# Optimization experiments

Measured on AMD Instinct MI355X. Metric: run time of the kernel, lower is better.

Reference implementation:

```python
import jax, jax.numpy as jnp
import numpy as np

B, S, D, H = 4, 2048, 1024, 16
DH = D // H
DFF = 4 * D
EPS = 1e-7


def _layernorm(x, scale, shift):
    # Note original quirk: (normalized + shift) * scale, biased variance, eps=1e-7
    m = jnp.mean(x, axis=-1, keepdims=True)
    v = jnp.mean((x - m) ** 2, axis=-1, keepdims=True)
    return ((x - m) / jnp.sqrt(v + EPS) + shift) * scale


def _gelu(x):
    c = jnp.sqrt(jnp.asarray(2.0 / jnp.pi, dtype=x.dtype))
    return 0.5 * x * (1.0 + jnp.tanh(c * (x + 0.044715 * x ** 3)))


def setup_inputs() -> dict:
    key = jax.random.key(0)
    ks = jax.random.split(key, 8)
    s = 0.02
    return {
        "x": jax.random.normal(ks[0], (B, S, D), jnp.float32),
        "Wq": jax.random.normal(ks[1], (D, D), jnp.float32) * s,
        "Wk": jax.random.normal(ks[2], (D, D), jnp.float32) * s,
        "Wv": jax.random.normal(ks[3], (D, D), jnp.float32) * s,
        "Wo": jax.random.normal(ks[4], (D, D), jnp.float32) * s,
        "bo": jnp.zeros((D,), jnp.float32),
        "W1": jax.random.normal(ks[5], (DFF, D), jnp.float32) * s,
        "b1": jnp.zeros((DFF,), jnp.float32),
        "W2": jax.random.normal(ks[6], (D, DFF), jnp.float32) * s,
        "b2": jnp.zeros((D,), jnp.float32),
        "ln1_scale": jnp.ones((D,), jnp.float32),
        "ln1_shift": jnp.zeros((D,), jnp.float32),
        "ln2_scale": jnp.ones((D,), jnp.float32),
        "ln2_shift": jnp.zeros((D,), jnp.float32),
    }


def reference(x, Wq, Wk, Wv, Wo, bo, W1, b1, W2, b2,
              ln1_scale, ln1_shift, ln2_scale, ln2_shift):
    b, s, d = x.shape
    h = _layernorm(x, ln1_scale, ln1_shift)
    # torch Linear: y = h @ W.T
    q = (h @ Wq.T).reshape(b, s, H, DH).transpose(0, 2, 1, 3)  # bhsd
    k = (h @ Wk.T).reshape(b, s, H, DH).transpose(0, 2, 1, 3)
    v = (h @ Wv.T).reshape(b, s, H, DH).transpose(0, 2, 1, 3)
    scores = jnp.einsum('bhqd,bhkd->bhqk', q, k) / jnp.sqrt(jnp.asarray(DH, x.dtype))
    causal = jnp.tril(jnp.ones((s, s), dtype=bool))
    scores = jnp.where(causal, scores, -jnp.inf)
    attn = jax.nn.softmax(scores, axis=-1)
    ctx = jnp.einsum('bhqk,bhkd->bhqd', attn, v)
    ctx = ctx.transpose(0, 2, 1, 3).reshape(b, s, d)
    attn_out = ctx @ Wo.T + bo
    x1 = x + attn_out  # residual (dropout is identity at eval / p effectively unused)
    h2 = _layernorm(x1, ln2_scale, ln2_shift)
    ff = _gelu(h2 @ W1.T + b1) @ W2.T + b2
    return x1 + ff
```

## Files before the change

kernel.cpp:

```cpp
#include <hip/hip_runtime.h>
#include <hip/hip_bf16.h>
#include <math.h>

typedef __bf16 bf16;
typedef __bf16 bf16x2_t __attribute__((ext_vector_type(2)));
typedef __bf16 bf16x4_t __attribute__((ext_vector_type(4)));
typedef __bf16 bf16x8_t __attribute__((ext_vector_type(8)));
typedef float  floatx4  __attribute__((ext_vector_type(4)));

#define DEVI static __device__ __forceinline__

constexpr int Bb = 4, Ss = 2048, Dd = 1024, Hh = 16, DHh = 64, DFFc = 4096;
constexpr int NTOK = Bb * Ss;
constexpr int NQKV = 3072;

DEVI void gld_lds16(const void* g, void* l) {
  __builtin_amdgcn_global_load_lds(
      (const __attribute__((address_space(1))) void*)g,
      (__attribute__((address_space(3))) void*)l, 16, 0, 0);
}

DEVI float gelu_f(float x) {
  const float c = 0.7978845608028654f;
  float t = tanhf(c * (x + 0.044715f * x * x * x));
  return 0.5f * x * (1.0f + t);
}

DEVI int xcd_lin(int lin, int nwg) {
  return (lin & 7) * (nwg >> 3) + (lin >> 3);
}

struct CastArgs {
  const float* src[6];
  bf16* dst[6];
  int n[6];
};
__global__ __launch_bounds__(256) void cast_w_kernel(CastArgs a) {
  const int which = blockIdx.y;
  const int idx = (blockIdx.x * 256 + threadIdx.x) * 4;
  if (idx >= a.n[which]) return;
  float4 v = *(const float4*)(a.src[which] + idx);
  bf16x4_t o = {(bf16)v.x, (bf16)v.y, (bf16)v.z, (bf16)v.w};
  *(bf16x4_t*)(a.dst[which] + idx) = o;
}

template <typename TIN>
__global__ __launch_bounds__(256) void ln_kernel(const TIN* __restrict__ x,
                                                 const float* __restrict__ sc,
                                                 const float* __restrict__ sh,
                                                 bf16* __restrict__ out) {
  __shared__ float rs[4], rs2[4];
  const int row = blockIdx.x, t = threadIdx.x;
  const TIN* xr = x + (size_t)row * Dd;
  float v[4];
  if constexpr (sizeof(TIN) == 2) {
    bf16x4_t tmp = *(const bf16x4_t*)((const bf16*)xr + t * 4);
#pragma unroll
    for (int i = 0; i < 4; i++) v[i] = (float)tmp[i];
  } else {
    float4 tmp = *(const float4*)((const float*)xr + t * 4);
    v[0] = tmp.x; v[1] = tmp.y; v[2] = tmp.z; v[3] = tmp.w;
  }
  float s = v[0] + v[1] + v[2] + v[3];
  float s2 = v[0] * v[0] + v[1] * v[1] + v[2] * v[2] + v[3] * v[3];
#pragma unroll
  for (int off = 1; off < 64; off <<= 1) {
    s += __shfl_xor(s, off);
    s2 += __shfl_xor(s2, off);
  }
  if ((t & 63) == 0) { rs[t >> 6] = s; rs2[t >> 6] = s2; }
  __syncthreads();
  float S1 = rs[0] + rs[1] + rs[2] + rs[3];
  float S2 = rs2[0] + rs2[1] + rs2[2] + rs2[3];
  float mean = S1 * (1.0f / Dd);
  float var = S2 * (1.0f / Dd) - mean * mean;
  float rinv = rsqrtf(var + 1e-7f);
#pragma unroll
  for (int i = 0; i < 4; i++) {
    int c = t * 4 + i;
    out[(size_t)row * Dd + c] = (bf16)(((v[i] - mean) * rinv + sh[c]) * sc[c]);
  }
}

template <int BN, int MODE>
__global__ __launch_bounds__(512, 2) void gemm8(const bf16* __restrict__ A,
                                                const bf16* __restrict__ Bw,
                                                const float* __restrict__ bias,
                                                const void* __restrict__ res,
                                                void* __restrict__ outp,
                                                int M, int N, int K) {
  constexpr int WARPS_N = (BN == 256) ? 4 : 2;
  constexpr int WR_H = (BN == 256) ? 128 : 64;
  constexpr int M_rep = WR_H / 16;
  constexpr int MPP = M_rep / 4;
  constexpr int NBCH = BN / 128;
  constexpr int BELEM = BN * 64;
  __shared__ bf16 lds[32768 + 2 * BELEM];

  const int tid = threadIdx.x;
  const int w = tid >> 6, lane = tid & 63;
  const int quad = lane >> 4, l16 = lane & 15;
  const int l7x8 = (lane & 7) << 3;
  const int wr = w / WARPS_N, wc = w % WARPS_N;

  const int gx = (int)gridDim.x;
  const int nwg = gx * (int)gridDim.y;
  const int lin = xcd_lin((int)blockIdx.y * gx + (int)blockIdx.x, nwg);
  const int m0 = (lin / gx) * 256;
  const int n0 = (lin % gx) * BN;

  const int s0 = w * 1024 + lane * 16;
  const int sr = s0 >> 7;
  const int sc = ((s0 ^ ((sr & 7) << 4)) & 127) >> 1;
  const int toff = w * 512 + lane * 8;

  const bf16* Ag[2][2];
  const bf16* Bg[NBCH][2];
#pragma unroll
  for (int h = 0; h < 2; h++)
#pragma unroll
    for (int j = 0; j < 2; j++)
      Ag[h][j] = A + (size_t)(m0 + h * 128 + sr + j * 64) * K + sc;
#pragma unroll
  for (int h = 0; h < NBCH; h++)
#pragma unroll
    for (int j = 0; j < 2; j++)
      Bg[h][j] = Bw + (size_t)(n0 + h * 128 + sr + j * 64) * K + sc;

  const int abase = (wr * WR_H + l16) * 64 + quad * 8;
  const int bbase = (wc * 64 + l16) * 64 + quad * 8;

  floatx4 acc[M_rep][4] = {};

#pragma unroll
  for (int h = 0; h < 2; h++)
#pragma unroll
    for (int j = 0; j < 2; j++)
      gld_lds16(Ag[h][j], lds + h * 8192 + j * 4096 + toff);
#pragma unroll
  for (int h = 0; h < NBCH; h++)
#pragma unroll
    for (int j = 0; j < 2; j++)
      gld_lds16(Bg[h][j], lds + 32768 + h * 8192 + j * 4096 + toff);
  asm volatile("s_waitcnt vmcnt(0)" ::: "memory");
  __builtin_amdgcn_s_barrier();
  __builtin_amdgcn_sched_barrier(0);

  const int NT = K >> 6;
  int koff = 64;
  for (int t = 0; t < NT; ++t) {
    const int q = t & 1;
    const int aq = q * 16384;
    const int bq = 32768 + q * BELEM;
    const int aqn = (q ^ 1) * 16384;
    const int bqn = 32768 + (q ^ 1) * BELEM;
    const bool st = (t + 1) < NT;

    bf16x8_t bfr[4][2];
#pragma unroll
    for (int p = 0; p < 4; ++p) {
      if (st) {
        if (p == 0) {
#pragma unroll
          for (int j = 0; j < 2; j++)
            gld_lds16(Ag[0][j] + koff, lds + aqn + j * 4096 + toff);
#pragma unroll
          for (int j = 0; j < 2; j++)
            gld_lds16(Bg[0][j] + koff, lds + bqn + j * 4096 + toff);
        }
        if (p == 1) {
#pragma unroll
          for (int j = 0; j < 2; j++)
            gld_lds16(Ag[1][j] + koff, lds + aqn + 8192 + j * 4096 + toff);
        }
        if (p == 2 && NBCH == 2) {
#pragma unroll
          for (int j = 0; j < 2; j++)
            gld_lds16(Bg[1][j] + koff, lds + bqn + 8192 + j * 4096 + toff);
        }
      }
      bf16x8_t af[MPP][2];
#pragma unroll
      for (int im = 0; im < MPP; ++im)
#pragma unroll
        for (int kk = 0; kk < 2; ++kk)
          af[im][kk] = *(const bf16x8_t*)(
              lds + aq + ((abase + (p * MPP + im) * 1024 + kk * 32) ^ l7x8));
      if (p == 0) {
#pragma unroll
        for (int j2 = 0; j2 < 4; ++j2)
#pragma unroll
          for (int kk = 0; kk < 2; ++kk)
            bfr[j2][kk] = *(const bf16x8_t*)(
                lds + bq + ((bbase + j2 * 1024 + kk * 32) ^ l7x8));
      }
      __builtin_amdgcn_s_barrier();
      __builtin_amdgcn_sched_barrier(0);
      __builtin_amdgcn_s_setprio(1);
#pragma unroll
      for (int im = 0; im < MPP; ++im)
#pragma unroll
        for (int j2 = 0; j2 < 4; ++j2)
#pragma unroll
          for (int kk = 0; kk < 2; ++kk)
            acc[p * MPP + im][j2] = __builtin_amdgcn_mfma_f32_16x16x32_bf16(
                af[im][kk], bfr[j2][kk], acc[p * MPP + im][j2], 0, 0, 0);
      __builtin_amdgcn_s_setprio(0);
      if (p < 3) {
        __builtin_amdgcn_s_barrier();
        __builtin_amdgcn_sched_barrier(0);
      }
    }
    asm volatile("s_waitcnt vmcnt(0)" ::: "memory");
    __builtin_amdgcn_sched_barrier(0);
    __builtin_amdgcn_s_barrier();
    __builtin_amdgcn_sched_barrier(0);
    if (st) koff += 64;
  }

#pragma unroll
  for (int i = 0; i < M_rep; ++i) {
    const int rbase = m0 + wr * WR_H + i * 16 + quad * 4;
#pragma unroll
    for (int j2 = 0; j2 < 4; ++j2) {
      const int col = n0 + wc * 64 + j2 * 16 + l16;
      float bv = 0.f;
      if constexpr (MODE == 1 || MODE == 2 || MODE == 3) bv = bias[col];
#pragma unroll
      for (int r = 0; r < 4; ++r) {
        const int row = rbase + r;
        float vacc = acc[i][j2][r] + bv;
        if constexpr (MODE == 0) {
          ((bf16*)outp)[(size_t)row * N + col] = (bf16)vacc;
        } else if constexpr (MODE == 1) {
          float xres = ((const float*)res)[(size_t)row * N + col];
          ((bf16*)outp)[(size_t)row * N + col] = (bf16)(xres + vacc);
        } else if constexpr (MODE == 2) {
          ((bf16*)outp)[(size_t)row * N + col] = (bf16)gelu_f(vacc);
        } else {
          float xres = (float)((const bf16*)res)[(size_t)row * N + col];
          ((float*)outp)[(size_t)row * N + col] = xres + vacc;
        }
      }
    }
  }
}

__global__ __launch_bounds__(256) void attn_kernel(const bf16* __restrict__ QKV,
                                                   bf16* __restrict__ ctx) {
  __shared__ bf16 Ks[64 * 72];
  __shared__ bf16 Vt[64 * 72];
  __shared__ bf16 Ps[4][16 * 72];

  const int tid = threadIdx.x;
  const int wave = tid >> 6, lane = tid & 63;
  const int quad = lane >> 4, l16 = lane & 15;
  const int lin = xcd_lin((int)blockIdx.y * 16 + (int)blockIdx.x, 16 * Bb * Hh);
  const int qb = lin & 15;
  const int bh = lin >> 4;
  const int bsel = bh >> 4, hsel = bh & 15;
  const size_t base = ((size_t)bsel * Ss) * NQKV + (size_t)hsel * 64;
  const bf16* Qp = QKV + base;
  const bf16* Kp = QKV + base + 1024;
  const bf16* Vp = QKV + base + 2048;

  const int kr0 = tid >> 3, kc0 = (tid & 7) * 8;
  const int vp2 = tid & 31, vs = tid >> 5;

  for (int t = 0; t < 2; t++) {
    const int qt = (t == 0) ? qb : 31 - qb;
    const int q0 = qt * 64;

    const int qrow = q0 + wave * 16 + l16;
    bf16x8_t qf0 = *(const bf16x8_t*)(Qp + (size_t)qrow * NQKV + quad * 8);
    bf16x8_t qf1 = *(const bf16x8_t*)(Qp + (size_t)qrow * NQKV + 32 + quad * 8);
#pragma unroll
    for (int i = 0; i < 8; i++) {
      qf0[i] = (bf16)((float)qf0[i] * 0.125f);
      qf1[i] = (bf16)((float)qf1[i] * 0.125f);
    }

    floatx4 o[4] = {};
    float l_i[4] = {0.f, 0.f, 0.f, 0.f};

    for (int kc = 0; kc < q0 + 64; kc += 64) {
      __syncthreads();
      *(bf16x8_t*)(Ks + kr0 * 72 + kc0) =
          *(const bf16x8_t*)(Kp + (size_t)(kc + kr0) * NQKV + kc0);
      *(bf16x8_t*)(Ks + (kr0 + 32) * 72 + kc0) =
          *(const bf16x8_t*)(Kp + (size_t)(kc + kr0 + 32) * NQKV + kc0);
      {
        const bf16* v0p = Vp + (size_t)(kc + 2 * vp2) * NQKV + vs * 8;
        bf16x8_t va = *(const bf16x8_t*)(v0p);
        bf16x8_t vb = *(const bf16x8_t*)(v0p + NQKV);
#pragma unroll
        for (int i = 0; i < 8; i++) {
          bf16x2_t p2 = {va[i], vb[i]};
          *(bf16x2_t*)(Vt + (vs * 8 + i) * 72 + 2 * vp2) = p2;
        }
      }
      __syncthreads();

      floatx4 sg[4];
      __builtin_amdgcn_s_setprio(1);
#pragma unroll
      for (int g = 0; g < 4; g++) {
        floatx4 s = {0.f, 0.f, 0.f, 0.f};
        bf16x8_t ka = *(const bf16x8_t*)(Ks + (g * 16 + l16) * 72 + quad * 8);
        bf16x8_t kb = *(const bf16x8_t*)(Ks + (g * 16 + l16) * 72 + 32 + quad * 8);
        s = __builtin_amdgcn_mfma_f32_16x16x32_bf16(qf0, ka, s, 0, 0, 0);
        s = __builtin_amdgcn_mfma_f32_16x16x32_bf16(qf1, kb, s, 0, 0, 0);
        sg[g] = s;
      }
      __builtin_amdgcn_s_setprio(0);

      bf16* pw = &Ps[wave][0];
#pragma unroll
      for (int r = 0; r < 4; r++) {
        const int rq = q0 + wave * 16 + quad * 4 + r;
        float p[4];
        float rsum = 0.f;
#pragma unroll
        for (int g = 0; g < 4; g++) {
          float v = (kc + g * 16 + l16 > rq) ? -1e30f : sg[g][r];
          p[g] = __expf(v);
          rsum += p[g];
        }
        rsum += __shfl_xor(rsum, 1);
        rsum += __shfl_xor(rsum, 2);
        rsum += __shfl_xor(rsum, 4);
        rsum += __shfl_xor(rsum, 8);
        l_i[r] += rsum;
#pragma unroll
        for (int g = 0; g < 4; g++)
          pw[(quad * 4 + r) * 72 + g * 16 + l16] = (bf16)p[g];
      }
      __syncthreads();

      bf16x8_t pf0 = *(const bf16x8_t*)(pw + l16 * 72 + quad * 8);
      bf16x8_t pf1 = *(const bf16x8_t*)(pw + l16 * 72 + 32 + quad * 8);
      __builtin_amdgcn_s_setprio(1);
#pragma unroll
      for (int nt = 0; nt < 4; nt++) {
        bf16x8_t vf0 = *(const bf16x8_t*)(Vt + (nt * 16 + l16) * 72 + quad * 8);
        bf16x8_t vf1 = *(const bf16x8_t*)(Vt + (nt * 16 + l16) * 72 + 32 + quad * 8);
        o[nt] = __builtin_amdgcn_mfma_f32_16x16x32_bf16(pf0, vf0, o[nt], 0, 0, 0);
        o[nt] = __builtin_amdgcn_mfma_f32_16x16x32_bf16(pf1, vf1, o[nt], 0, 0, 0);
      }
      __builtin_amdgcn_s_setprio(0);
    }

#pragma unroll
    for (int nt = 0; nt < 4; nt++)
#pragma unroll
      for (int r = 0; r < 4; r++) {
        const int rq = q0 + wave * 16 + quad * 4 + r;
        size_t a = ((size_t)bsel * Ss + rq) * Dd + (size_t)hsel * DHh + nt * 16 + l16;
        ctx[a] = (bf16)(o[nt][r] / l_i[r]);
      }
  }
}

extern "C" void kernel_launch(void* const* d_in, const int* in_sizes, int n_in,
                              void* d_out, int out_size, void* d_ws, size_t ws_size,
                              hipStream_t stream) {
  (void)in_sizes; (void)n_in; (void)out_size; (void)ws_size;
  const float* x = (const float*)d_in[0];
  const float* Wq = (const float*)d_in[1];
  const float* Wk = (const float*)d_in[2];
  const float* Wv = (const float*)d_in[3];
  const float* Wo = (const float*)d_in[4];
  const float* bo = (const float*)d_in[5];
  const float* W1 = (const float*)d_in[6];
  const float* b1 = (const float*)d_in[7];
  const float* W2 = (const float*)d_in[8];
  const float* b2 = (const float*)d_in[9];
  const float* ln1s = (const float*)d_in[10];
  const float* ln1b = (const float*)d_in[11];
  const float* ln2s = (const float*)d_in[12];
  const float* ln2b = (const float*)d_in[13];

  char* wsb = (char*)d_ws;
  const size_t MB = 1024 * 1024;
  bf16* Wqb = (bf16*)(wsb);
  bf16* Wkb = (bf16*)(wsb + 2 * MB);
  bf16* Wvb = (bf16*)(wsb + 4 * MB);
  bf16* Wob = (bf16*)(wsb + 6 * MB);
  bf16* W1b = (bf16*)(wsb + 8 * MB);
  bf16* W2b = (bf16*)(wsb + 16 * MB);
  bf16* h   = (bf16*)(wsb + 24 * MB);
  bf16* qkv = (bf16*)(wsb + 40 * MB);
  bf16* ctx = (bf16*)(wsb + 88 * MB);
  bf16* x1  = (bf16*)(wsb + 104 * MB);
  bf16* h2  = ctx;
  bf16* ff1 = h;

  dim3 blk(256, 1, 1);
  dim3 blk8(512, 1, 1);

  CastArgs ca;
  ca.src[0] = Wq; ca.src[1] = Wk; ca.src[2] = Wv; ca.src[3] = Wo;
  ca.src[4] = W1; ca.src[5] = W2;
  ca.dst[0] = Wqb; ca.dst[1] = Wkb; ca.dst[2] = Wvb; ca.dst[3] = Wob;
  ca.dst[4] = W1b; ca.dst[5] = W2b;
  ca.n[0] = ca.n[1] = ca.n[2] = ca.n[3] = Dd * Dd;
  ca.n[4] = ca.n[5] = Dd * DFFc;
  cast_w_kernel<<<dim3((Dd * DFFc) / (256 * 4), 6, 1), blk, 0, stream>>>(ca);

  ln_kernel<float><<<dim3(NTOK, 1, 1), blk, 0, stream>>>(x, ln1s, ln1b, h);
  gemm8<128, 0><<<dim3(24, NTOK / 256, 1), blk8, 0, stream>>>(h, Wqb, nullptr, nullptr,
                                                              qkv, NTOK, NQKV, Dd);
  attn_kernel<<<dim3(16, Bb * Hh, 1), blk, 0, stream>>>(qkv, ctx);
  gemm8<128, 1><<<dim3(8, NTOK / 256, 1), blk8, 0, stream>>>(ctx, Wob, bo, x, x1,
                                                             NTOK, Dd, Dd);
  ln_kernel<bf16><<<dim3(NTOK, 1, 1), blk, 0, stream>>>(x1, ln2s, ln2b, h2);
  gemm8<256, 2><<<dim3(16, NTOK / 256, 1), blk8, 0, stream>>>(h2, W1b, b1, nullptr, ff1,
                                                              NTOK, DFFc, Dd);
  gemm8<128, 3><<<dim3(8, NTOK / 256, 1), blk8, 0, stream>>>(ff1, W2b, b2, x1,
                                                             (float*)d_out, NTOK, Dd, DFFc);
}
```

Measured before the change: 521.9 us.

## Triple-buffer GEMM k-loop and prefetch next K/V tile in attention

The GEMM moves to a three-stage LDS ring buffer with a fixed 256x128 tile, issuing loads two k-steps ahead and waiting with a partial vmcnt instead of draining every iteration. The FF1 GEMM now uses this narrower tile too. In attention, the next K/V tile is loaded into registers while the current tile computes, and the causal mask is applied only on the diagonal tile. The larger LDS footprint can lower blocks per CU.

```diff
diff --git a/kernel.cpp b/kernel.cpp
--- a/kernel.cpp
+++ b/kernel.cpp
@@ -82,32 +82,30 @@
   }
 }
 
-template <int BN, int MODE>
+template <int MODE>
 __global__ __launch_bounds__(512, 2) void gemm8(const bf16* __restrict__ A,
                                                 const bf16* __restrict__ Bw,
                                                 const float* __restrict__ bias,
                                                 const void* __restrict__ res,
                                                 void* __restrict__ outp,
                                                 int M, int N, int K) {
-  constexpr int WARPS_N = (BN == 256) ? 4 : 2;
-  constexpr int WR_H = (BN == 256) ? 128 : 64;
-  constexpr int M_rep = WR_H / 16;
-  constexpr int MPP = M_rep / 4;
-  constexpr int NBCH = BN / 128;
-  constexpr int BELEM = BN * 64;
-  __shared__ bf16 lds[32768 + 2 * BELEM];
+  constexpr int ABUF = 16384;
+  constexpr int BBUF = 8192;
+  __shared__ bf16 lds[3 * (ABUF + BBUF)];
+  bf16* Ab = lds;
+  bf16* Bb = lds + 3 * ABUF;
 
   const int tid = threadIdx.x;
   const int w = tid >> 6, lane = tid & 63;
   const int quad = lane >> 4, l16 = lane & 15;
   const int l7x8 = (lane & 7) << 3;
-  const int wr = w / WARPS_N, wc = w % WARPS_N;
+  const int wr = w >> 1, wc = w & 1;
 
   const int gx = (int)gridDim.x;
   const int nwg = gx * (int)gridDim.y;
   const int lin = xcd_lin((int)blockIdx.y * gx + (int)blockIdx.x, nwg);
   const int m0 = (lin / gx) * 256;
-  const int n0 = (lin % gx) * BN;
+  const int n0 = (lin % gx) * 128;
 
   const int s0 = w * 1024 + lane * 16;
   const int sr = s0 >> 7;
@@ -115,112 +113,90 @@
   const int toff = w * 512 + lane * 8;
 
   const bf16* Ag[2][2];
-  const bf16* Bg[NBCH][2];
+  const bf16* Bg[2];
 #pragma unroll
   for (int h = 0; h < 2; h++)
 #pragma unroll
     for (int j = 0; j < 2; j++)
-      Ag[h][j] = A + (size_t)(m0 + h * 128 + sr + j * 64) * K + sc;
-#pragma unroll
-  for (int h = 0; h < NBCH; h++)
+      Ag[h][j] = A + (size_t)(m0 + h * 128 + j * 64 + sr) * K + sc;
+#pragma unroll
+  for (int j = 0; j < 2; j++)
+    Bg[j] = Bw + (size_t)(n0 + j * 64 + sr) * K + sc;
+
+  auto issue = [&](int kofs, int s) {
+#pragma unroll
+    for (int h = 0; h < 2; h++)
+#pragma unroll
+      for (int j = 0; j < 2; j++)
+        gld_lds16(Ag[h][j] + kofs, Ab + s * ABUF + h * 8192 + j * 4096 + toff);
 #pragma unroll
     for (int j = 0; j < 2; j++)
-      Bg[h][j] = Bw + (size_t)(n0 + h * 128 + sr + j * 64) * K + sc;
-
-  const int abase = (wr * WR_H + l16) * 64 + quad * 8;
+      gld_lds16(Bg[j] + kofs, Bb + s * BBUF + j * 4096 + toff);
+  };
+
+  const int abase = (wr * 64 + l16) * 64 + quad * 8;
   const int bbase = (wc * 64 + l16) * 64 + quad * 8;
 
-  floatx4 acc[M_rep][4] = {};
-
-#pragma unroll
-  for (int h = 0; h < 2; h++)
-#pragma unroll
-    for (int j = 0; j < 2; j++)
-      gld_lds16(Ag[h][j], lds + h * 8192 + j * 4096 + toff);
-#pragma unroll
-  for (int h = 0; h < NBCH; h++)
-#pragma unroll
-    for (int j = 0; j < 2; j++)
-      gld_lds16(Bg[h][j], lds + 32768 + h * 8192 + j * 4096 + toff);
-  asm volatile("s_waitcnt vmcnt(0)" ::: "memory");
-  __builtin_amdgcn_s_barrier();
-  __builtin_amdgcn_sched_barrier(0);
+  floatx4 acc[4][4] = {};
 
   const int NT = K >> 6;
-  int koff = 64;
+  issue(0, 0);
+  issue(64, 1);
+
   for (int t = 0; t < NT; ++t) {
-    const int q = t & 1;
-    const int aq = q * 16384;
-    const int bq = 32768 + q * BELEM;
-    const int aqn = (q ^ 1) * 16384;
-    const int bqn = 32768 + (q ^ 1) * BELEM;
-    const bool st = (t + 1) < NT;
-
+    const int s = t % 3;
+    if (t < NT - 1) {
+      asm volatile("s_waitcnt vmcnt(6)" ::: "memory");
+    } else {
+      asm volatile("s_waitcnt vmcnt(0)" ::: "memory");
+    }
+    __builtin_amdgcn_sched_barrier(0);
+    __builtin_amdgcn_s_barrier();
+    __builtin_amdgcn_sched_barrier(0);
+    if (t + 2 < NT) issue((t + 2) * 64, (t + 2) % 3);
+
+    const bf16* aB = Ab + s * ABUF;
+    const bf16* bB = Bb + s * BBUF;
     bf16x8_t bfr[4][2];
 #pragma unroll
-    for (int p = 0; p < 4; ++p) {
-      if (st) {
-        if (p == 0) {
-#pragma unroll
-          for (int j = 0; j < 2; j++)
-            gld_lds16(Ag[0][j] + koff, lds + aqn + j * 4096 + toff);
-#pragma unroll
-          for (int j = 0; j < 2; j++)
-            gld_lds16(Bg[0][j] + koff, lds + bqn + j * 4096 + toff);
-        }
-        if (p == 1) {
-#pragma unroll
-          for (int j = 0; j < 2; j++)
-            gld_lds16(Ag[1][j] + koff, lds + aqn + 8192 + j * 4096 + toff);
-        }
-        if (p == 2 && NBCH == 2) {
-#pragma unroll
-          for (int j = 0; j < 2; j++)
-            gld_lds16(Bg[1][j] + koff, lds + bqn + 8192 + j * 4096 + toff);
-        }
-      }
-      bf16x8_t af[MPP][2];
-#pragma unroll
-      for (int im = 0; im < MPP; ++im)
+    for (int p = 0; p < 2; ++p) {
+      bf16x8_t af[2][2];
+#pragma unroll
+      for (int im = 0; im < 2; ++im)
 #pragma unroll
         for (int kk = 0; kk < 2; ++kk)
           af[im][kk] = *(const bf16x8_t*)(
-              lds + aq + ((abase + (p * MPP + im) * 1024 + kk * 32) ^ l7x8));
+              aB + ((abase + (p * 2 + im) * 1024 + kk * 32) ^ l7x8));
       if (p == 0) {
 #pragma unroll
         for (int j2 = 0; j2 < 4; ++j2)
 #pragma unroll
           for (int kk = 0; kk < 2; ++kk)
             bfr[j2][kk] = *(const bf16x8_t*)(
-                lds + bq + ((bbase + j2 * 1024 + kk * 32) ^ l7x8));
+                bB + ((bbase + j2 * 1024 + kk * 32) ^ l7x8));
       }
       __builtin_amdgcn_s_barrier();
       __builtin_amdgcn_sched_barrier(0);
       __builtin_amdgcn_s_setprio(1);
 #pragma unroll
-      for (int im = 0; im < MPP; ++im)
+      for (int im = 0; im < 2; ++im)
 #pragma unroll
         for (int j2 = 0; j2 < 4; ++j2)
 #pragma unroll
           for (int kk = 0; kk < 2; ++kk)
-            acc[p * MPP + im][j2] = __builtin_amdgcn_mfma_f32_16x16x32_bf16(
-                af[im][kk], bfr[j2][kk], acc[p * MPP + im][j2], 0, 0, 0);
+            acc[p * 2 + im][j2] = __builtin_amdgcn_mfma_f32_16x16x32_bf16(
+                af[im][kk], bfr[j2][kk], acc[p * 2 + im][j2], 0, 0, 0);
       __builtin_amdgcn_s_setprio(0);
-      if (p < 3) {
+      if (p == 0) {
         __builtin_amdgcn_s_barrier();
         __builtin_amdgcn_sched_barrier(0);
       }
     }
-    asm volatile("s_waitcnt vmcnt(0)" ::: "memory");
-    __builtin_amdgcn_sched_barrier(0);
-    __builtin_amdgcn_s_barrier();
-    __builtin_amdgcn_sched_barrier(0);
-    if (st) koff += 64;
-  }
-
-#pragma unroll
-  for (int i = 0; i < M_rep; ++i) {
-    const int rbase = m0 + wr * WR_H + i * 16 + quad * 4;
+  }
+
+#pragma unroll
+  for (int i = 0; i < 4; ++i) {
+    const int rbase = m0 + wr * 64 + i * 16 + quad * 4;
 #pragma unroll
     for (int j2 = 0; j2 < 4; ++j2) {
       const int col = n0 + wc * 64 + j2 * 16 + l16;
@@ -283,23 +259,36 @@
     floatx4 o[4] = {};
     float l_i[4] = {0.f, 0.f, 0.f, 0.f};
 
-    for (int kc = 0; kc < q0 + 64; kc += 64) {
+    {
+      bf16x8_t k0 = *(const bf16x8_t*)(Kp + (size_t)kr0 * NQKV + kc0);
+      bf16x8_t k1 = *(const bf16x8_t*)(Kp + (size_t)(kr0 + 32) * NQKV + kc0);
+      const bf16* v0p = Vp + (size_t)(2 * vp2) * NQKV + vs * 8;
+      bf16x8_t va = *(const bf16x8_t*)(v0p);
+      bf16x8_t vb = *(const bf16x8_t*)(v0p + NQKV);
+      *(bf16x8_t*)(Ks + kr0 * 72 + kc0) = k0;
+      *(bf16x8_t*)(Ks + (kr0 + 32) * 72 + kc0) = k1;
+#pragma unroll
+      for (int i = 0; i < 8; i++) {
+        bf16x2_t p2 = {va[i], vb[i]};
+        *(bf16x2_t*)(Vt + (vs * 8 + i) * 72 + 2 * vp2) = p2;
+      }
       __syncthreads();
-      *(bf16x8_t*)(Ks + kr0 * 72 + kc0) =
-          *(const bf16x8_t*)(Kp + (size_t)(kc + kr0) * NQKV + kc0);
-      *(bf16x8_t*)(Ks + (kr0 + 32) * 72 + kc0) =
-          *(const bf16x8_t*)(Kp + (size_t)(kc + kr0 + 32) * NQKV + kc0);
-      {
-        const bf16* v0p = Vp + (size_t)(kc + 2 * vp2) * NQKV + vs * 8;
-        bf16x8_t va = *(const bf16x8_t*)(v0p);
-        bf16x8_t vb = *(const bf16x8_t*)(v0p + NQKV);
-#pragma unroll
-        for (int i = 0; i < 8; i++) {
-          bf16x2_t p2 = {va[i], vb[i]};
-          *(bf16x2_t*)(Vt + (vs * 8 + i) * 72 + 2 * vp2) = p2;
-        }
-      }
-      __syncthreads();
+    }
+
+    const int ntiles = qt + 1;
+    for (int it = 0; it < ntiles; ++it) {
+      const int kc = it * 64;
+      const bool more = (it + 1) < ntiles;
+
+      bf16x8_t nk0, nk1, nva, nvb;
+      if (more) {
+        const int kn = kc + 64;
+        nk0 = *(const bf16x8_t*)(Kp + (size_t)(kn + kr0) * NQKV + kc0);
+        nk1 = *(const bf16x8_t*)(Kp + (size_t)(kn + kr0 + 32) * NQKV + kc0);
+        const bf16* v0p = Vp + (size_t)(kn + 2 * vp2) * NQKV + vs * 8;
+        nva = *(const bf16x8_t*)(v0p);
+        nvb = *(const bf16x8_t*)(v0p + NQKV);
+      }
 
       floatx4 sg[4];
       __builtin_amdgcn_s_setprio(1);
@@ -315,27 +304,48 @@
       __builtin_amdgcn_s_setprio(0);
 
       bf16* pw = &Ps[wave][0];
-#pragma unroll
-      for (int r = 0; r < 4; r++) {
-        const int rq = q0 + wave * 16 + quad * 4 + r;
-        float p[4];
-        float rsum = 0.f;
-#pragma unroll
-        for (int g = 0; g < 4; g++) {
-          float v = (kc + g * 16 + l16 > rq) ? -1e30f : sg[g][r];
-          p[g] = __expf(v);
-          rsum += p[g];
+      const bool diag = (kc == q0);
+      if (diag) {
+#pragma unroll
+        for (int r = 0; r < 4; r++) {
+          const int rq = q0 + wave * 16 + quad * 4 + r;
+          float p[4];
+          float rsum = 0.f;
+#pragma unroll
+          for (int g = 0; g < 4; g++) {
+            float v = (kc + g * 16 + l16 > rq) ? -1e30f : sg[g][r];
+            p[g] = __expf(v);
+            rsum += p[g];
+          }
+          rsum += __shfl_xor(rsum, 1);
+          rsum += __shfl_xor(rsum, 2);
+          rsum += __shfl_xor(rsum, 4);
+          rsum += __shfl_xor(rsum, 8);
+          l_i[r] += rsum;
+#pragma unroll
+          for (int g = 0; g < 4; g++)
+            pw[(quad * 4 + r) * 72 + g * 16 + l16] = (bf16)p[g];
         }
-        rsum += __shfl_xor(rsum, 1);
-        rsum += __shfl_xor(rsum, 2);
-        rsum += __shfl_xor(rsum, 4);
-        rsum += __shfl_xor(rsum, 8);
-        l_i[r] += rsum;
-#pragma unroll
-        for (int g = 0; g < 4; g++)
-          pw[(quad * 4 + r) * 72 + g * 16 + l16] = (bf16)p[g];
-      }
-      __syncthreads();
+      } else {
+#pragma unroll
+        for (int r = 0; r < 4; r++) {
+          float p[4];
+          float rsum = 0.f;
+#pragma unroll
+          for (int g = 0; g < 4; g++) {
+            p[g] = __expf(sg[g][r]);
+            rsum += p[g];
+          }
+          rsum += __shfl_xor(rsum, 1);
+          rsum += __shfl_xor(rsum, 2);
+          rsum += __shfl_xor(rsum, 4);
+          rsum += __shfl_xor(rsum, 8);
+          l_i[r] += rsum;
+#pragma unroll
+          for (int g = 0; g < 4; g++)
+            pw[(quad * 4 + r) * 72 + g * 16 + l16] = (bf16)p[g];
+        }
+      }
 
       bf16x8_t pf0 = *(const bf16x8_t*)(pw + l16 * 72 + quad * 8);
       bf16x8_t pf1 = *(const bf16x8_t*)(pw + l16 * 72 + 32 + quad * 8);
@@ -348,6 +358,18 @@
         o[nt] = __builtin_amdgcn_mfma_f32_16x16x32_bf16(pf1, vf1, o[nt], 0, 0, 0);
       }
       __builtin_amdgcn_s_setprio(0);
+
+      __syncthreads();
+      if (more) {
+        *(bf16x8_t*)(Ks + kr0 * 72 + kc0) = nk0;
+        *(bf16x8_t*)(Ks + (kr0 + 32) * 72 + kc0) = nk1;
+#pragma unroll
+        for (int i = 0; i < 8; i++) {
+          bf16x2_t p2 = {nva[i], nvb[i]};
+          *(bf16x2_t*)(Vt + (vs * 8 + i) * 72 + 2 * vp2) = p2;
+        }
+        __syncthreads();
+      }
     }
 
 #pragma unroll
@@ -408,14 +430,14 @@
   cast_w_kernel<<<dim3((Dd * DFFc) / (256 * 4), 6, 1), blk, 0, stream>>>(ca);
 
   ln_kernel<float><<<dim3(NTOK, 1, 1), blk, 0, stream>>>(x, ln1s, ln1b, h);
-  gemm8<128, 0><<<dim3(24, NTOK / 256, 1), blk8, 0, stream>>>(h, Wqb, nullptr, nullptr,
-                                                              qkv, NTOK, NQKV, Dd);
+  gemm8<0><<<dim3(24, NTOK / 256, 1), blk8, 0, stream>>>(h, Wqb, nullptr, nullptr,
+                                                         qkv, NTOK, NQKV, Dd);
   attn_kernel<<<dim3(16, Bb * Hh, 1), blk, 0, stream>>>(qkv, ctx);
-  gemm8<128, 1><<<dim3(8, NTOK / 256, 1), blk8, 0, stream>>>(ctx, Wob, bo, x, x1,
-                                                             NTOK, Dd, Dd);
+  gemm8<1><<<dim3(8, NTOK / 256, 1), blk8, 0, stream>>>(ctx, Wob, bo, x, x1,
+                                                        NTOK, Dd, Dd);
   ln_kernel<bf16><<<dim3(NTOK, 1, 1), blk, 0, stream>>>(x1, ln2s, ln2b, h2);
-  gemm8<256, 2><<<dim3(16, NTOK / 256, 1), blk8, 0, stream>>>(h2, W1b, b1, nullptr, ff1,
-                                                              NTOK, DFFc, Dd);
-  gemm8<128, 3><<<dim3(8, NTOK / 256, 1), blk8, 0, stream>>>(ff1, W2b, b2, x1,
-                                                             (float*)d_out, NTOK, Dd, DFFc);
-}
+  gemm8<2><<<dim3(32, NTOK / 256, 1), blk8, 0, stream>>>(h2, W1b, b1, nullptr, ff1,
+                                                         NTOK, DFFc, Dd);
+  gemm8<3><<<dim3(8, NTOK / 256, 1), blk8, 0, stream>>>(ff1, W2b, b2, x1,
+                                                        (float*)d_out, NTOK, Dd, DFFc);
+}
```

After: 530.4 us. About the same (+1.6%).
